# Optimization experiments

Hardware: AMD Instinct MI355X
Metric: run time of the kernel (lower is better)

## Reference

```python
import jax, jax.numpy as jnp
import numpy as np
import math

H_DIM = 1024
N_HEADS = 16
B, T = 2, 2048


def setup_inputs() -> dict:
    key = jax.random.key(0)
    ks = jax.random.split(key, 9)
    scale = 1.0 / math.sqrt(H_DIM)
    x = jax.random.normal(ks[0], (B, T, H_DIM), dtype=jnp.float32)
    Wq = jax.random.normal(ks[1], (H_DIM, H_DIM), dtype=jnp.float32) * scale
    Wk = jax.random.normal(ks[2], (H_DIM, H_DIM), dtype=jnp.float32) * scale
    Wv = jax.random.normal(ks[3], (H_DIM, H_DIM), dtype=jnp.float32) * scale
    Wp = jax.random.normal(ks[4], (H_DIM, H_DIM), dtype=jnp.float32) * scale
    bq = jnp.zeros((H_DIM,), dtype=jnp.float32)
    bk = jnp.zeros((H_DIM,), dtype=jnp.float32)
    bv = jnp.zeros((H_DIM,), dtype=jnp.float32)
    bp = jnp.zeros((H_DIM,), dtype=jnp.float32)
    return {"x": x, "Wq": Wq, "bq": bq, "Wk": Wk, "bk": bk,
            "Wv": Wv, "bv": bv, "Wp": Wp, "bp": bp}


def _attention(x, Wq, bq, Wk, bk, Wv, bv, Wp, bp):
    Bx, Tx, C = x.shape
    N = N_HEADS
    D = C // N
    # torch Linear: x @ W.T + b
    q = (x @ Wq.T + bq).reshape(Bx, Tx, N, D).transpose(0, 2, 1, 3)  # [B,N,T,D]
    k = (x @ Wk.T + bk).reshape(Bx, Tx, N, D).transpose(0, 2, 1, 3)
    v = (x @ Wv.T + bv).reshape(Bx, Tx, N, D).transpose(0, 2, 1, 3)
    scores = jnp.einsum('bntd,bnsd->bnts', q, k) / math.sqrt(D)  # [B,N,T,T]
    causal = jnp.tril(jnp.ones((Tx, Tx), dtype=bool))
    scores = jnp.where(causal[None, None], scores, -jnp.inf)
    probs = jax.nn.softmax(scores, axis=-1)
    attn = jnp.einsum('bnts,bnsd->bntd', probs, v)  # [B,N,T,D]
    attn = attn.transpose(0, 2, 1, 3).reshape(Bx, Tx, C)
    return attn @ Wp.T + bp


def reference(x, Wq, bq, Wk, bk, Wv, bv, Wp, bp):
    return _attention(x, Wq, bq, Wk, bk, Wv, bv, Wp, bp)
```

## Files before the change

kernel.cpp:

```cpp
#include <hip/hip_runtime.h>
#include <hip/hip_bf16.h>
#include <math.h>

#define TSEQ 2048
#define CDIM 1024
#define NHEADS 16
#define DHEAD 64
#define BSZ 2
#define MROWS (BSZ * TSEQ)
#define SCALE_Q 0.18033688f

typedef __attribute__((ext_vector_type(8))) short short8;
typedef __attribute__((ext_vector_type(4))) short short4v;
typedef __attribute__((ext_vector_type(4))) float f32x4;

__device__ inline f32x4 mfma16(short8 a, short8 b, f32x4 c) {
    return __builtin_amdgcn_mfma_f32_16x16x32_bf16(a, b, c, 0, 0, 0);
}

__device__ inline short f2bf(float f) {
    __hip_bfloat16 h = __float2bfloat16(f);
    return __builtin_bit_cast(short, h);
}

__global__ __launch_bounds__(256) void convx_kernel(const float* __restrict__ x,
                                                    short* __restrict__ xb) {
    size_t off = (size_t)(blockIdx.x * 256 + threadIdx.x) * 8;
    float4 a = *(const float4*)(x + off);
    float4 b = *(const float4*)(x + off + 4);
    short8 h;
    h[0] = f2bf(a.x); h[1] = f2bf(a.y); h[2] = f2bf(a.z); h[3] = f2bf(a.w);
    h[4] = f2bf(b.x); h[5] = f2bf(b.y); h[6] = f2bf(b.z); h[7] = f2bf(b.w);
    *(short8*)(xb + off) = h;
}

__global__ __launch_bounds__(256, 3) void gemm_qkv(
    const short* __restrict__ xb, const float* __restrict__ Wq,
    const float* __restrict__ Wk, const float* __restrict__ Wv,
    const float* __restrict__ bq, const float* __restrict__ bk,
    const float* __restrict__ bv, short* __restrict__ qws,
    short* __restrict__ kws, short* __restrict__ vtws) {
    __shared__ __attribute__((aligned(16))) short a_lds[128][72];
    __shared__ __attribute__((aligned(16))) short b_lds[128][72];

    const int tid = threadIdx.x;
    const int lane = tid & 63;
    const int wv = tid >> 6;
    const int wr = wv >> 1, wc = wv & 1;
    const int l15 = lane & 15, l4 = lane >> 4;

    const int hw = blockIdx.x + 32 * blockIdx.y;
    const int work = (hw & 7) * 96 + (hw >> 3);
    const int mbase = (work & 31) * 128;
    const int wy = work >> 5;
    const int which = wy >> 3;
    const int nbase = (wy & 7) * 128;
    const float* Wf = which == 0 ? Wq : (which == 1 ? Wk : Wv);
    const float* bias = which == 0 ? bq : (which == 1 ? bk : bv);

    f32x4 acc[4][4];
#pragma unroll
    for (int i = 0; i < 4; ++i)
#pragma unroll
        for (int j = 0; j < 4; ++j) acc[i][j] = f32x4{0.f, 0.f, 0.f, 0.f};

    const int ar = tid >> 3;
    const int ag = (tid & 7) * 8;
    const int br = tid >> 4;
    const int bg = (tid & 15) * 4;
    const short* aptr = xb + (size_t)(mbase + ar) * CDIM + ag;
    const float* bptr = Wf + (size_t)(nbase + br) * CDIM + bg;

    short8 apre[4];
    float4 bpre[8];
#pragma unroll
    for (int it = 0; it < 4; ++it)
        apre[it] = *(const short8*)(aptr + (size_t)(32 * it) * CDIM);
#pragma unroll
    for (int it = 0; it < 8; ++it)
        bpre[it] = *(const float4*)(bptr + (size_t)(16 * it) * CDIM);

    for (int k0 = 0; k0 < CDIM; k0 += 64) {
        __syncthreads();
#pragma unroll
        for (int it = 0; it < 4; ++it)
            *(short8*)&a_lds[ar + 32 * it][ag] = apre[it];
#pragma unroll
        for (int it = 0; it < 8; ++it) {
            short4v h;
            h.x = f2bf(bpre[it].x); h.y = f2bf(bpre[it].y);
            h.z = f2bf(bpre[it].z); h.w = f2bf(bpre[it].w);
            *(short4v*)&b_lds[br + 16 * it][bg] = h;
        }
        __syncthreads();
        if (k0 + 64 < CDIM) {
#pragma unroll
            for (int it = 0; it < 4; ++it)
                apre[it] = *(const short8*)(aptr + (size_t)(32 * it) * CDIM + k0 + 64);
#pragma unroll
            for (int it = 0; it < 8; ++it)
                bpre[it] = *(const float4*)(bptr + (size_t)(16 * it) * CDIM + k0 + 64);
        }

#pragma unroll
        for (int kk = 0; kk < 2; ++kk) {
            short8 af[4], bfr[4];
#pragma unroll
            for (int i = 0; i < 4; ++i)
                af[i] = *(const short8*)&a_lds[wr * 64 + i * 16 + l15][kk * 32 + l4 * 8];
#pragma unroll
            for (int j = 0; j < 4; ++j)
                bfr[j] = *(const short8*)&b_lds[wc * 64 + j * 16 + l15][kk * 32 + l4 * 8];
#pragma unroll
            for (int i = 0; i < 4; ++i)
#pragma unroll
                for (int j = 0; j < 4; ++j)
                    acc[i][j] = mfma16(af[i], bfr[j], acc[i][j]);
        }
    }

    if (which < 2) {
        short* dst = which == 0 ? qws : kws;
        const float scale = which == 0 ? SCALE_Q : 1.0f;
#pragma unroll
        for (int i = 0; i < 4; ++i) {
            int mrow = mbase + wr * 64 + i * 16 + l4 * 4;
#pragma unroll
            for (int j = 0; j < 4; ++j) {
                int o = nbase + wc * 64 + j * 16 + l15;
                int n = o >> 6, d = o & 63;
                float bval = bias[o];
#pragma unroll
                for (int r = 0; r < 4; ++r) {
                    int mm = mrow + r;
                    int bb = mm >> 11;
                    int t = mm & (TSEQ - 1);
                    dst[(((size_t)bb * NHEADS + n) * TSEQ + t) * DHEAD + d] =
                        f2bf((acc[i][j][r] + bval) * scale);
                }
            }
        }
    } else {
#pragma unroll
        for (int i = 0; i < 4; ++i) {
            int mrow = mbase + wr * 64 + i * 16 + l4 * 4;
            int bb = mrow >> 11;
            int t = mrow & (TSEQ - 1);
#pragma unroll
            for (int j = 0; j < 4; ++j) {
                int o = nbase + wc * 64 + j * 16 + l15;
                int n = o >> 6, d = o & 63;
                float bval = bias[o];
                short4v h4;
#pragma unroll
                for (int r = 0; r < 4; ++r) h4[r] = f2bf(acc[i][j][r] + bval);
                *(short4v*)&vtws[(((size_t)bb * NHEADS + n) * DHEAD + d) * TSEQ + t] = h4;
            }
        }
    }
}

__global__ __launch_bounds__(256) void gemm_p(
    const short* __restrict__ attn, const float* __restrict__ Wp,
    const float* __restrict__ bp, float* __restrict__ out) {
    __shared__ __attribute__((aligned(16))) short a_lds[64][40];
    __shared__ __attribute__((aligned(16))) short b_lds[128][40];

    const int tid = threadIdx.x;
    const int lane = tid & 63;
    const int wv = tid >> 6;
    const int wr = wv >> 1, wc = wv & 1;
    const int l15 = lane & 15, l4 = lane >> 4;

    const int hw = blockIdx.x + 64 * blockIdx.y;
    const int work = (hw & 7) * 64 + (hw >> 3);
    const int mbase = (work & 63) * 64;
    const int nbase = (work >> 6) * 128;

    f32x4 acc[2][4];
#pragma unroll
    for (int i = 0; i < 2; ++i)
#pragma unroll
        for (int j = 0; j < 4; ++j) acc[i][j] = f32x4{0.f, 0.f, 0.f, 0.f};

    const int arow = tid >> 2;
    const int acol = (tid & 3) * 8;
    const int brow = tid >> 3;
    const int bcol = (tid & 7) * 4;
    const short* aptr = attn + (size_t)(mbase + arow) * CDIM + acol;
    const float* bptr = Wp + (size_t)(nbase + brow) * CDIM + bcol;

    short8 apre;
    float4 bpre[4];
    apre = *(const short8*)(aptr);
#pragma unroll
    for (int it = 0; it < 4; ++it)
        bpre[it] = *(const float4*)(bptr + (size_t)(it * 32) * CDIM);

    for (int k0 = 0; k0 < CDIM; k0 += 32) {
        __syncthreads();
        *(short8*)&a_lds[arow][acol] = apre;
#pragma unroll
        for (int it = 0; it < 4; ++it) {
            short4v h;
            h.x = f2bf(bpre[it].x); h.y = f2bf(bpre[it].y);
            h.z = f2bf(bpre[it].z); h.w = f2bf(bpre[it].w);
            *(short4v*)&b_lds[brow + it * 32][bcol] = h;
        }
        __syncthreads();
        if (k0 + 32 < CDIM) {
            apre = *(const short8*)(aptr + k0 + 32);
#pragma unroll
            for (int it = 0; it < 4; ++it)
                bpre[it] = *(const float4*)(bptr + (size_t)(it * 32) * CDIM + k0 + 32);
        }

        short8 af[2], bfr[4];
#pragma unroll
        for (int i = 0; i < 2; ++i)
            af[i] = *(const short8*)&a_lds[wr * 32 + i * 16 + l15][l4 * 8];
#pragma unroll
        for (int j = 0; j < 4; ++j)
            bfr[j] = *(const short8*)&b_lds[wc * 64 + j * 16 + l15][l4 * 8];
#pragma unroll
        for (int i = 0; i < 2; ++i)
#pragma unroll
            for (int j = 0; j < 4; ++j)
                acc[i][j] = mfma16(af[i], bfr[j], acc[i][j]);
    }

#pragma unroll
    for (int i = 0; i < 2; ++i) {
        int mrow = mbase + wr * 32 + i * 16 + l4 * 4;
#pragma unroll
        for (int j = 0; j < 4; ++j) {
            int o = nbase + wc * 64 + j * 16 + l15;
            float bval = bp[o];
#pragma unroll
            for (int r = 0; r < 4; ++r)
                out[(size_t)(mrow + r) * CDIM + o] = acc[i][j][r] + bval;
        }
    }
}

__global__ __launch_bounds__(256) void attn_kernel(
    const short* __restrict__ q, const short* __restrict__ k,
    const short* __restrict__ vt, short* __restrict__ attn_out) {
    __shared__ __attribute__((aligned(16))) short k_lds[64][64];
    __shared__ __attribute__((aligned(16))) short vt_lds[64][64];
    __shared__ __attribute__((aligned(16))) short p_lds[4][16][80];

    const int tid = threadIdx.x;
    const int w = tid >> 6;
    const int lane = tid & 63;
    const int l15 = lane & 15;
    const int l4 = lane >> 4;
    const int h = blockIdx.x;
    const int qtile = gridDim.y - 1 - blockIdx.y;
    const int qb = qtile * 64;
    const int wrow0 = qb + w * 16;

    short8 qf[2];
#pragma unroll
    for (int kh = 0; kh < 2; ++kh)
        qf[kh] = *(const short8*)(q + ((size_t)h * TSEQ + wrow0 + l15) * DHEAD +
                                  kh * 32 + l4 * 8);

    float l_run[4];
    f32x4 o_acc[4];
#pragma unroll
    for (int r = 0; r < 4; ++r) l_run[r] = 0.f;
#pragma unroll
    for (int dt = 0; dt < 4; ++dt) o_acc[dt] = f32x4{0.f, 0.f, 0.f, 0.f};

    const int ntiles = qtile + 1;
    const int srow = tid >> 3;
    const int sgrp = tid & 7;

    short8 kpre[2], vpre[2];
#pragma unroll
    for (int it = 0; it < 2; ++it) {
        int row = srow + it * 32;
        kpre[it] = *(const short8*)(k + ((size_t)h * TSEQ + row) * DHEAD + sgrp * 8);
        vpre[it] = *(const short8*)(vt + ((size_t)h * DHEAD + row) * TSEQ + sgrp * 8);
    }

    for (int kvt = 0; kvt < ntiles; ++kvt) {
        const int kvbase = kvt * 64;
        __syncthreads();
#pragma unroll
        for (int it = 0; it < 2; ++it) {
            int row = srow + it * 32;
            int gs = sgrp ^ (row & 7);
            *(short8*)&k_lds[row][gs * 8] = kpre[it];
            *(short8*)&vt_lds[row][gs * 8] = vpre[it];
        }
        __syncthreads();
        if (kvt + 1 < ntiles) {
            int kvb2 = kvbase + 64;
#pragma unroll
            for (int it = 0; it < 2; ++it) {
                int row = srow + it * 32;
                kpre[it] = *(const short8*)(k + ((size_t)h * TSEQ + kvb2 + row) * DHEAD + sgrp * 8);
                vpre[it] = *(const short8*)(vt + ((size_t)h * DHEAD + row) * TSEQ + kvb2 + sgrp * 8);
            }
        }

        f32x4 s[4];
#pragma unroll
        for (int jt = 0; jt < 4; ++jt) {
            int row = jt * 16 + l15;
            int sw = row & 7;
            short8 kf0 = *(const short8*)&k_lds[row][(l4 ^ sw) * 8];
            short8 kf1 = *(const short8*)&k_lds[row][((4 + l4) ^ sw) * 8];
            f32x4 a = f32x4{0.f, 0.f, 0.f, 0.f};
            a = mfma16(qf[0], kf0, a);
            a = mfma16(qf[1], kf1, a);
            s[jt] = a;
        }

        const bool needmask = (kvbase + 63 > wrow0);
#pragma unroll
        for (int r = 0; r < 4; ++r) {
            int qrow = wrow0 + l4 * 4 + r;
            float lp = 0.f;
#pragma unroll
            for (int jt = 0; jt < 4; ++jt) {
                float x = s[jt][r];
                if (needmask && (kvbase + jt * 16 + l15 > qrow)) x = -INFINITY;
                float e = __builtin_amdgcn_exp2f(x);
                unsigned int eb = __builtin_bit_cast(unsigned int, e);
                p_lds[w][l4 * 4 + r][jt * 16 + l15] = (short)(eb >> 16);
                lp += __builtin_bit_cast(float, eb & 0xffff0000u);
            }
            l_run[r] += lp;
        }

        short8 pa0 = *(const short8*)&p_lds[w][l15][l4 * 8];
        short8 pa1 = *(const short8*)&p_lds[w][l15][32 + l4 * 8];
#pragma unroll
        for (int dt = 0; dt < 4; ++dt) {
            int row = dt * 16 + l15;
            int sw = row & 7;
            short8 vf0 = *(const short8*)&vt_lds[row][(l4 ^ sw) * 8];
            short8 vf1 = *(const short8*)&vt_lds[row][((4 + l4) ^ sw) * 8];
            o_acc[dt] = mfma16(pa0, vf0, o_acc[dt]);
            o_acc[dt] = mfma16(pa1, vf1, o_acc[dt]);
        }
    }

#pragma unroll
    for (int r = 0; r < 4; ++r) {
        float l = l_run[r];
#pragma unroll
        for (int mk = 1; mk < 16; mk <<= 1) l += __shfl_xor(l, mk);
        l_run[r] = 1.0f / l;
    }
    const int b = h >> 4, n = h & 15;
#pragma unroll
    for (int dt = 0; dt < 4; ++dt) {
#pragma unroll
        for (int r = 0; r < 4; ++r) {
            int t = wrow0 + l4 * 4 + r;
            attn_out[((size_t)b * TSEQ + t) * CDIM + n * DHEAD + dt * 16 + l15] =
                f2bf(o_acc[dt][r] * l_run[r]);
        }
    }
}

extern "C" void kernel_launch(void* const* d_in, const int* in_sizes, int n_in,
                              void* d_out, int out_size, void* d_ws, size_t ws_size,
                              hipStream_t stream) {
    const float* x  = (const float*)d_in[0];
    const float* Wq = (const float*)d_in[1];
    const float* bq = (const float*)d_in[2];
    const float* Wk = (const float*)d_in[3];
    const float* bk = (const float*)d_in[4];
    const float* Wv = (const float*)d_in[5];
    const float* bv = (const float*)d_in[6];
    const float* Wp = (const float*)d_in[7];
    const float* bp = (const float*)d_in[8];

    char* ws = (char*)d_ws;
    const size_t SZ = (size_t)MROWS * CDIM * sizeof(short);
    short* qws  = (short*)(ws);
    short* kws  = (short*)(ws + SZ);
    short* vtws = (short*)(ws + 2 * SZ);
    short* xb   = (short*)(ws + 3 * SZ);
    short* attn = xb;

    convx_kernel<<<2048, 256, 0, stream>>>(x, xb);
    gemm_qkv<<<dim3(MROWS / 128, 24), 256, 0, stream>>>(xb, Wq, Wk, Wv, bq, bk, bv,
                                                         qws, kws, vtws);
    attn_kernel<<<dim3(BSZ * NHEADS, TSEQ / 64), 256, 0, stream>>>(qws, kws, vtws, attn);
    gemm_p<<<dim3(MROWS / 64, CDIM / 128), 256, 0, stream>>>(attn, Wp, bp, (float*)d_out);
}
```

Before: 119.1 us.

## Process 128 query rows per attention block, two 16-row tiles per wave

Each attention block now covers 128 query rows, so each wave computes two 16-row query subtiles against every K/V tile loaded into LDS. K/V fragments are reused across both subtiles, which halves global and LDS traffic for K/V per query row and halves the number of blocks. Waves whose rows lie entirely before a KV tile skip its compute, but they still join the loads and barriers, so load across waves is uneven near the diagonal. The trade-off is more registers per wave and fewer blocks (512), which may lower occupancy and parallelism.

Result: slower. 126.8 us (+6.5%).

```diff
diff --git a/kernel.cpp b/kernel.cpp
--- a/kernel.cpp
+++ b/kernel.cpp
@@ -248,7 +248,7 @@
     const short* __restrict__ vt, short* __restrict__ attn_out) {
     __shared__ __attribute__((aligned(16))) short k_lds[64][64];
     __shared__ __attribute__((aligned(16))) short vt_lds[64][64];
-    __shared__ __attribute__((aligned(16))) short p_lds[4][16][80];
+    __shared__ __attribute__((aligned(16))) short p_lds[4][32][80];
 
     const int tid = threadIdx.x;
     const int w = tid >> 6;
@@ -257,23 +257,29 @@
     const int l4 = lane >> 4;
     const int h = blockIdx.x;
     const int qtile = gridDim.y - 1 - blockIdx.y;
-    const int qb = qtile * 64;
-    const int wrow0 = qb + w * 16;
-
-    short8 qf[2];
-#pragma unroll
-    for (int kh = 0; kh < 2; ++kh)
-        qf[kh] = *(const short8*)(q + ((size_t)h * TSEQ + wrow0 + l15) * DHEAD +
-                                  kh * 32 + l4 * 8);
-
-    float l_run[4];
-    f32x4 o_acc[4];
-#pragma unroll
-    for (int r = 0; r < 4; ++r) l_run[r] = 0.f;
-#pragma unroll
-    for (int dt = 0; dt < 4; ++dt) o_acc[dt] = f32x4{0.f, 0.f, 0.f, 0.f};
-
-    const int ntiles = qtile + 1;
+    const int qb = qtile * 128;
+    const int wrow0 = qb + w * 32;
+
+    short8 qf[2][2];
+#pragma unroll
+    for (int rt = 0; rt < 2; ++rt)
+#pragma unroll
+        for (int kh = 0; kh < 2; ++kh)
+            qf[rt][kh] = *(const short8*)(q + ((size_t)h * TSEQ + wrow0 + rt * 16 + l15) * DHEAD +
+                                          kh * 32 + l4 * 8);
+
+    float l_run[2][4];
+    f32x4 o_acc[2][4];
+#pragma unroll
+    for (int rt = 0; rt < 2; ++rt)
+#pragma unroll
+        for (int r = 0; r < 4; ++r) l_run[rt][r] = 0.f;
+#pragma unroll
+    for (int rt = 0; rt < 2; ++rt)
+#pragma unroll
+        for (int dt = 0; dt < 4; ++dt) o_acc[rt][dt] = f32x4{0.f, 0.f, 0.f, 0.f};
+
+    const int ntiles = 2 * qtile + 2;
     const int srow = tid >> 3;
     const int sgrp = tid & 7;
 
@@ -305,65 +311,82 @@
                 vpre[it] = *(const short8*)(vt + ((size_t)h * DHEAD + row) * TSEQ + kvb2 + sgrp * 8);
             }
         }
-
-        f32x4 s[4];
+        if (kvbase > wrow0 + 31) continue;
+
+        f32x4 s[2][4];
 #pragma unroll
         for (int jt = 0; jt < 4; ++jt) {
             int row = jt * 16 + l15;
             int sw = row & 7;
             short8 kf0 = *(const short8*)&k_lds[row][(l4 ^ sw) * 8];
             short8 kf1 = *(const short8*)&k_lds[row][((4 + l4) ^ sw) * 8];
-            f32x4 a = f32x4{0.f, 0.f, 0.f, 0.f};
-            a = mfma16(qf[0], kf0, a);
-            a = mfma16(qf[1], kf1, a);
-            s[jt] = a;
+#pragma unroll
+            for (int rt = 0; rt < 2; ++rt) {
+                f32x4 a = f32x4{0.f, 0.f, 0.f, 0.f};
+                a = mfma16(qf[rt][0], kf0, a);
+                a = mfma16(qf[rt][1], kf1, a);
+                s[rt][jt] = a;
+            }
         }
 
         const bool needmask = (kvbase + 63 > wrow0);
 #pragma unroll
-        for (int r = 0; r < 4; ++r) {
-            int qrow = wrow0 + l4 * 4 + r;
-            float lp = 0.f;
-#pragma unroll
-            for (int jt = 0; jt < 4; ++jt) {
-                float x = s[jt][r];
-                if (needmask && (kvbase + jt * 16 + l15 > qrow)) x = -INFINITY;
-                float e = __builtin_amdgcn_exp2f(x);
-                unsigned int eb = __builtin_bit_cast(unsigned int, e);
-                p_lds[w][l4 * 4 + r][jt * 16 + l15] = (short)(eb >> 16);
-                lp += __builtin_bit_cast(float, eb & 0xffff0000u);
-            }
-            l_run[r] += lp;
-        }
-
-        short8 pa0 = *(const short8*)&p_lds[w][l15][l4 * 8];
-        short8 pa1 = *(const short8*)&p_lds[w][l15][32 + l4 * 8];
+        for (int rt = 0; rt < 2; ++rt) {
+#pragma unroll
+            for (int r = 0; r < 4; ++r) {
+                int qrow = wrow0 + rt * 16 + l4 * 4 + r;
+                float lp = 0.f;
+#pragma unroll
+                for (int jt = 0; jt < 4; ++jt) {
+                    float x = s[rt][jt][r];
+                    if (needmask && (kvbase + jt * 16 + l15 > qrow)) x = -INFINITY;
+                    float e = __builtin_amdgcn_exp2f(x);
+                    unsigned int eb = __builtin_bit_cast(unsigned int, e);
+                    p_lds[w][rt * 16 + l4 * 4 + r][jt * 16 + l15] = (short)(eb >> 16);
+                    lp += __builtin_bit_cast(float, eb & 0xffff0000u);
+                }
+                l_run[rt][r] += lp;
+            }
+        }
+
+        short8 pa[2][2];
+#pragma unroll
+        for (int rt = 0; rt < 2; ++rt) {
+            pa[rt][0] = *(const short8*)&p_lds[w][rt * 16 + l15][l4 * 8];
+            pa[rt][1] = *(const short8*)&p_lds[w][rt * 16 + l15][32 + l4 * 8];
+        }
 #pragma unroll
         for (int dt = 0; dt < 4; ++dt) {
             int row = dt * 16 + l15;
             int sw = row & 7;
             short8 vf0 = *(const short8*)&vt_lds[row][(l4 ^ sw) * 8];
             short8 vf1 = *(const short8*)&vt_lds[row][((4 + l4) ^ sw) * 8];
-            o_acc[dt] = mfma16(pa0, vf0, o_acc[dt]);
-            o_acc[dt] = mfma16(pa1, vf1, o_acc[dt]);
-        }
-    }
-
-#pragma unroll
-    for (int r = 0; r < 4; ++r) {
-        float l = l_run[r];
-#pragma unroll
-        for (int mk = 1; mk < 16; mk <<= 1) l += __shfl_xor(l, mk);
-        l_run[r] = 1.0f / l;
-    }
+#pragma unroll
+            for (int rt = 0; rt < 2; ++rt) {
+                o_acc[rt][dt] = mfma16(pa[rt][0], vf0, o_acc[rt][dt]);
+                o_acc[rt][dt] = mfma16(pa[rt][1], vf1, o_acc[rt][dt]);
+            }
+        }
+    }
+
     const int b = h >> 4, n = h & 15;
 #pragma unroll
-    for (int dt = 0; dt < 4; ++dt) {
+    for (int rt = 0; rt < 2; ++rt) {
 #pragma unroll
         for (int r = 0; r < 4; ++r) {
-            int t = wrow0 + l4 * 4 + r;
-            attn_out[((size_t)b * TSEQ + t) * CDIM + n * DHEAD + dt * 16 + l15] =
-                f2bf(o_acc[dt][r] * l_run[r]);
+            float l = l_run[rt][r];
+#pragma unroll
+            for (int mk = 1; mk < 16; mk <<= 1) l += __shfl_xor(l, mk);
+            l_run[rt][r] = 1.0f / l;
+        }
+#pragma unroll
+        for (int dt = 0; dt < 4; ++dt) {
+#pragma unroll
+            for (int r = 0; r < 4; ++r) {
+                int t = wrow0 + rt * 16 + l4 * 4 + r;
+                attn_out[((size_t)b * TSEQ + t) * CDIM + n * DHEAD + dt * 16 + l15] =
+                    f2bf(o_acc[rt][dt][r] * l_run[rt][r]);
+            }
         }
     }
 }
@@ -392,6 +415,6 @@
     convx_kernel<<<2048, 256, 0, stream>>>(x, xb);
     gemm_qkv<<<dim3(MROWS / 128, 24), 256, 0, stream>>>(xb, Wq, Wk, Wv, bq, bk, bv,
                                                          qws, kws, vtws);
-    attn_kernel<<<dim3(BSZ * NHEADS, TSEQ / 64), 256, 0, stream>>>(qws, kws, vtws, attn);
+    attn_kernel<<<dim3(BSZ * NHEADS, TSEQ / 128), 256, 0, stream>>>(qws, kws, vtws, attn);
     gemm_p<<<dim3(MROWS / 64, CDIM / 128), 256, 0, stream>>>(attn, Wp, bp, (float*)d_out);
 }
```
